# Kernel tuning notes

Hardware: AMD Instinct MI355X
Metric: run time of the kernel (lower is better)

## Reference

```python
import jax, jax.numpy as jnp
import numpy as np

HEADS = 8
DIM_HEAD = 64
SCALE = DIM_HEAD ** -0.5


def setup_inputs() -> dict:
    key = jax.random.key(0)
    ks = jax.random.split(key, 6)
    B, N, D = 1, 4096, 640
    INNER = HEADS * DIM_HEAD  # 512
    s = lambda fan_in: 1.0 / np.sqrt(fan_in)
    return {
        "x": jax.random.normal(ks[0], (B, N, D), dtype=jnp.float32),
        "Wq": jax.random.normal(ks[1], (D, INNER), dtype=jnp.float32) * s(D),
        "Wk": jax.random.normal(ks[2], (D, INNER), dtype=jnp.float32) * s(D),
        "Wv": jax.random.normal(ks[3], (D, INNER), dtype=jnp.float32) * s(D),
        "Wo": jax.random.normal(ks[4], (INNER, D), dtype=jnp.float32) * s(INNER),
        "bo": jnp.zeros((D,), dtype=jnp.float32),
    }


def reference(x, Wq, Wk, Wv, Wo, bo):
    B, N, _ = x.shape
    h, d = HEADS, DIM_HEAD
    # self-attention: context = x
    q = (x @ Wq).reshape(B, N, h, d).transpose(0, 2, 1, 3)  # [B,h,N,d]
    k = (x @ Wk).reshape(B, N, h, d).transpose(0, 2, 1, 3)
    v = (x @ Wv).reshape(B, N, h, d).transpose(0, 2, 1, 3)
    sim = jnp.einsum('bhid,bhjd->bhij', q, k) * SCALE  # [B,h,N,N]
    attn = jax.nn.softmax(sim, axis=-1)
    out = jnp.einsum('bhij,bhjd->bhid', attn, v)  # [B,h,N,d]
    out = out.transpose(0, 2, 1, 3).reshape(B, N, h * d)  # [B,N,inner]
    return out @ Wo + bo  # dropout p=0.0 is identity
```

## Files before the change

kernel.cpp:

```cpp
#include <hip/hip_runtime.h>
#include <math.h>

#define NSEQ   4096
#define DMODEL 640
#define NHEAD  8
#define DHEAD  64
#define INNER  512
#define KVSPLIT 2

typedef _Float16 f16;
typedef _Float16 f16x8 __attribute__((ext_vector_type(8)));
typedef _Float16 f16x4 __attribute__((ext_vector_type(4)));
typedef float    f32x4 __attribute__((ext_vector_type(4)));

#define MFMA16(a, b, c) __builtin_amdgcn_mfma_f32_16x16x32_f16((a), (b), (c), 0, 0, 0)

#define QSCALE 0.18033688011112042f

__device__ __forceinline__ void gl16(const f16* g, f16* l) {
    __builtin_amdgcn_global_load_lds(
        (const __attribute__((address_space(1))) unsigned int*)g,
        (__attribute__((address_space(3))) unsigned int*)l, 16, 0, 0);
}

__global__ __launch_bounds__(256) void cvt_x(const float* __restrict__ x,
                                             f16* __restrict__ xh) {
    int i = (blockIdx.x * 256 + threadIdx.x) * 8;
    float4 a = *(const float4*)&x[i];
    float4 b = *(const float4*)&x[i + 4];
    f16x8 o = {(f16)a.x, (f16)a.y, (f16)a.z, (f16)a.w,
               (f16)b.x, (f16)b.y, (f16)b.z, (f16)b.w};
    *(f16x8*)&xh[i] = o;
}

__global__ __launch_bounds__(256) void transpose_cvtW(
    const float* __restrict__ Wq, const float* __restrict__ Wk,
    const float* __restrict__ Wv, const float* __restrict__ Wo,
    f16* __restrict__ WTq, f16* __restrict__ WTk, f16* __restrict__ WTv,
    f16* __restrict__ WoT) {
    __shared__ __align__(16) f16 T[64][72];
    const int bz = blockIdx.z;
    const float* src = bz == 0 ? Wq : bz == 1 ? Wk : bz == 2 ? Wv : Wo;
    f16* dst = bz == 0 ? WTq : bz == 1 ? WTk : bz == 2 ? WTv : WoT;
    const int R = (bz < 3) ? DMODEL : INNER;
    const int C = (bz < 3) ? INNER : DMODEL;
    const int c0 = blockIdx.x * 64, r0 = blockIdx.y * 64;
    if (c0 >= C || r0 >= R) return;
    const int t = threadIdx.x;
    {
        int r = t >> 2, cb = (t & 3) * 16;
#pragma unroll
        for (int i = 0; i < 16; i += 4) {
            float4 v = *(const float4*)&src[(size_t)(r0 + r) * C + c0 + cb + i];
            T[cb + i + 0][r] = (f16)v.x;
            T[cb + i + 1][r] = (f16)v.y;
            T[cb + i + 2][r] = (f16)v.z;
            T[cb + i + 3][r] = (f16)v.w;
        }
    }
    __syncthreads();
    {
        int c = t >> 2, rb = (t & 3) * 16;
        f16* d = dst + (size_t)(c0 + c) * R + r0 + rb;
        *(f16x8*)d = *(const f16x8*)&T[c][rb];
        *(f16x8*)(d + 8) = *(const f16x8*)&T[c][rb + 8];
    }
}

__global__ __launch_bounds__(256) void qkv_gemm16(
    const f16* __restrict__ xh,
    const f16* __restrict__ WTq, const f16* __restrict__ WTk,
    const f16* __restrict__ WTv,
    f16* __restrict__ q16, f16* __restrict__ k16, f16* __restrict__ vT16)
{
    __shared__ __align__(16) f16 S[12288];
    f16* Xs = S;
    f16* Ws = S + 8192;

    const int bx = blockIdx.x;
    const int by = blockIdx.y;
    const int bz = blockIdx.z;
    const f16* WT = (bz == 0) ? WTq : (bz == 1) ? WTk : WTv;

    const int tid = threadIdx.x;
    const int w = tid >> 6, lane = tid & 63;
    const int lr = lane & 15, lc = lane >> 4;
    const int srow8 = lane >> 3;
    const int le = 8 * ((lane & 7) ^ srow8);
    const int swz0 = 8 * (lc ^ (lr & 7));
    const int swz1 = 8 * ((lc + 4) ^ (lr & 7));
    const int m0 = by * 128, n0 = bx * 64;

    f32x4 acc[2][4] = {};

    for (int s = 0; s < DMODEL / 64; ++s) {
        const int k0 = s * 64;
#pragma unroll
        for (int c = 0; c < 4; ++c) {
            const int cc = 4 * w + c;
            gl16(xh + (size_t)(m0 + cc * 8 + srow8) * DMODEL + k0 + le,
                 &Xs[cc * 512]);
        }
#pragma unroll
        for (int c = 0; c < 2; ++c) {
            const int cc = 2 * w + c;
            gl16(WT + (size_t)(n0 + cc * 8 + srow8) * DMODEL + k0 + le,
                 &Ws[cc * 512]);
        }
        __syncthreads();
        f16x8 a0[2], a1[2];
#pragma unroll
        for (int g = 0; g < 2; ++g) {
            const int row = 32 * w + 16 * g + lr;
            a0[g] = *(const f16x8*)&Xs[row * 64 + swz0];
            a1[g] = *(const f16x8*)&Xs[row * 64 + swz1];
        }
#pragma unroll
        for (int nt = 0; nt < 4; ++nt) {
            f16x8 b0 = *(const f16x8*)&Ws[(nt * 16 + lr) * 64 + swz0];
            f16x8 b1 = *(const f16x8*)&Ws[(nt * 16 + lr) * 64 + swz1];
#pragma unroll
            for (int g = 0; g < 2; ++g)
                acc[g][nt] = MFMA16(a1[g], b1, MFMA16(a0[g], b0, acc[g][nt]));
        }
        __syncthreads();
    }

    const float sc = (bz == 0) ? QSCALE : 1.0f;
    if (bz < 2) {
#pragma unroll
        for (int g = 0; g < 2; ++g)
#pragma unroll
            for (int nt = 0; nt < 4; ++nt)
#pragma unroll
                for (int r = 0; r < 4; ++r)
                    S[(32 * w + 16 * g + 4 * lc + r) * 72 + nt * 16 + lr] =
                        (f16)(acc[g][nt][r] * sc);
        __syncthreads();
        f16* ob = ((bz == 0) ? q16 : k16) + (size_t)bx * NSEQ * DHEAD;
#pragma unroll
        for (int p = 0; p < 2; ++p) {
            const int rr = p * 64 + (tid >> 2), cb = (tid & 3) * 16;
            f16* dst = ob + (size_t)(m0 + rr) * DHEAD + cb;
            *(f16x8*)dst = *(const f16x8*)&S[rr * 72 + cb];
            *(f16x8*)(dst + 8) = *(const f16x8*)&S[rr * 72 + cb + 8];
        }
    } else {
#pragma unroll
        for (int g = 0; g < 2; ++g)
#pragma unroll
            for (int nt = 0; nt < 4; ++nt)
#pragma unroll
                for (int r = 0; r < 4; ++r)
                    S[(nt * 16 + lr) * 136 + 32 * w + 16 * g + 4 * lc + r] =
                        (f16)acc[g][nt][r];
        __syncthreads();
        const int rr = tid >> 2, cb = (tid & 3) * 32;
        f16* dst = vT16 + ((size_t)bx * DHEAD + rr) * NSEQ + m0 + cb;
        *(f16x8*)dst        = *(const f16x8*)&S[rr * 136 + cb];
        *(f16x8*)(dst + 8)  = *(const f16x8*)&S[rr * 136 + cb + 8];
        *(f16x8*)(dst + 16) = *(const f16x8*)&S[rr * 136 + cb + 16];
        *(f16x8*)(dst + 24) = *(const f16x8*)&S[rr * 136 + cb + 24];
    }
}

__global__ __launch_bounds__(256, 2) void attn_fwd(
    const f16* __restrict__ q16, const f16* __restrict__ k16,
    const f16* __restrict__ vT16, f16* __restrict__ Opart,
    float* __restrict__ Ml)
{
    __shared__ __align__(16) f16 KsB[2][4096];
    __shared__ __align__(16) f16 VtB[2][4096];
    __shared__ __align__(16) f16 Ps[8192];

    const int lin = blockIdx.x + 32 * blockIdx.y + 256 * blockIdx.z;
    const int h  = lin & 7;
    const int qb = (lin >> 3) & 31;
    const int sp = lin >> 8;

    const int tid = threadIdx.x;
    const int w = tid >> 6, lane = tid & 63;
    const int lr = lane & 15, lc = lane >> 4;
    const int srow8 = lane >> 3;
    const int le = 8 * ((lane & 7) ^ srow8);
    const int swz0 = 8 * (lc ^ (lr & 7));
    const int swz1 = 8 * ((lc + 4) ^ (lr & 7));

    const f16* kp = k16 + ((size_t)h * NSEQ + sp * (NSEQ / KVSPLIT)) * DHEAD;
    const f16* vp = vT16 + (size_t)h * DHEAD * NSEQ + sp * (NSEQ / KVSPLIT);

    f16x8 qf[2][2];
#pragma unroll
    for (int g = 0; g < 2; ++g) {
        const f16* qp = q16 +
            ((size_t)h * NSEQ + qb * 128 + 32 * w + 16 * g + lr) * DHEAD;
        qf[g][0] = *(const f16x8*)&qp[lc * 8];
        qf[g][1] = *(const f16x8*)&qp[32 + lc * 8];
    }

    float m_run[2] = {-INFINITY, -INFINITY}, l_run[2] = {0.f, 0.f};
    f32x4 o[2][4] = {};

#pragma unroll
    for (int c = 0; c < 2; ++c) {
        const int cc = 2 * w + c;
        gl16(kp + (size_t)(cc * 8 + srow8) * DHEAD + le, &KsB[0][cc * 512]);
        gl16(vp + (size_t)(cc * 8 + srow8) * NSEQ + le, &VtB[0][cc * 512]);
    }
    __syncthreads();

    const int NT = NSEQ / KVSPLIT / 64;
    for (int kt = 0; kt < NT; ++kt) {
        const int cur = kt & 1;
        if (kt < NT - 1) {
            const int nb = cur ^ 1;
#pragma unroll
            for (int c = 0; c < 2; ++c) {
                const int cc = 2 * w + c;
                gl16(kp + (size_t)((kt + 1) * 64 + cc * 8 + srow8) * DHEAD + le,
                     &KsB[nb][cc * 512]);
                gl16(vp + (size_t)(cc * 8 + srow8) * NSEQ + (kt + 1) * 64 + le,
                     &VtB[nb][cc * 512]);
            }
        }

        f32x4 s[2][4];
        const f32x4 z4 = {0.f, 0.f, 0.f, 0.f};
#pragma unroll
        for (int t = 0; t < 4; ++t) {
            f16x8 ka = *(const f16x8*)&KsB[cur][(t * 16 + lr) * 64 + swz0];
            f16x8 kb = *(const f16x8*)&KsB[cur][(t * 16 + lr) * 64 + swz1];
#pragma unroll
            for (int g = 0; g < 2; ++g)
                s[g][t] = MFMA16(kb, qf[g][1], MFMA16(ka, qf[g][0], z4));
        }

        float pm[2];
#pragma unroll
        for (int g = 0; g < 2; ++g) {
            float m = s[g][0][0];
#pragma unroll
            for (int t = 0; t < 4; ++t)
#pragma unroll
                for (int r = 0; r < 4; ++r) m = fmaxf(m, s[g][t][r]);
            m = fmaxf(m, __shfl_xor(m, 16));
            m = fmaxf(m, __shfl_xor(m, 32));
            pm[g] = m;
        }
        if (__any((pm[0] > m_run[0]) | (pm[1] > m_run[1]))) {
#pragma unroll
            for (int g = 0; g < 2; ++g) {
                const float mn = fmaxf(m_run[g], pm[g]);
                const float al = __builtin_amdgcn_exp2f(m_run[g] - mn);
                m_run[g] = mn;
                l_run[g] *= al;
#pragma unroll
                for (int dt = 0; dt < 4; ++dt) o[g][dt] *= al;
            }
        }
#pragma unroll
        for (int g = 0; g < 2; ++g) {
            float ps = 0.f;
#pragma unroll
            for (int t = 0; t < 4; ++t)
#pragma unroll
                for (int r = 0; r < 4; ++r) {
                    s[g][t][r] = __builtin_amdgcn_exp2f(s[g][t][r] - m_run[g]);
                    ps += s[g][t][r];
                }
            ps += __shfl_xor(ps, 16);
            ps += __shfl_xor(ps, 32);
            l_run[g] += ps;
        }

#pragma unroll
        for (int g = 0; g < 2; ++g) {
            const int row = 32 * w + 16 * g + lr;
#pragma unroll
            for (int t = 0; t < 4; ++t) {
                f16x4 pk = {(f16)s[g][t][0], (f16)s[g][t][1],
                            (f16)s[g][t][2], (f16)s[g][t][3]};
                const int col = (16 * t + 4 * lc) ^ ((lr & 7) << 3);
                *(f16x4*)&Ps[row * 64 + col] = pk;
            }
        }

        f16x8 pb[2][2];
#pragma unroll
        for (int g = 0; g < 2; ++g) {
            const int row = 32 * w + 16 * g + lr;
            pb[g][0] = *(const f16x8*)&Ps[row * 64 + swz0];
            pb[g][1] = *(const f16x8*)&Ps[row * 64 + swz1];
        }
#pragma unroll
        for (int dt = 0; dt < 4; ++dt) {
            f16x8 va0 = *(const f16x8*)&VtB[cur][(dt * 16 + lr) * 64 + swz0];
            f16x8 va1 = *(const f16x8*)&VtB[cur][(dt * 16 + lr) * 64 + swz1];
#pragma unroll
            for (int g = 0; g < 2; ++g)
                o[g][dt] = MFMA16(va1, pb[g][1], MFMA16(va0, pb[g][0], o[g][dt]));
        }
        __syncthreads();
    }

#pragma unroll
    for (int g = 0; g < 2; ++g) {
        const float linv = 1.0f / l_run[g];
        const size_t qg = (size_t)qb * 128 + 32 * w + 16 * g + lr;
        f16* ob = Opart + (((size_t)(sp * 8 + h)) * NSEQ + qg) * DHEAD;
#pragma unroll
        for (int dt = 0; dt < 4; ++dt) {
            f16x4 ov = {(f16)(o[g][dt][0] * linv), (f16)(o[g][dt][1] * linv),
                        (f16)(o[g][dt][2] * linv), (f16)(o[g][dt][3] * linv)};
            *(f16x4*)&ob[dt * 16 + 4 * lc] = ov;
        }
        if (lc == 0) {
            float2 ml = make_float2(m_run[g], l_run[g]);
            *(float2*)&Ml[(((size_t)(sp * 8 + h)) * NSEQ + qg) * 2] = ml;
        }
    }
}

__global__ __launch_bounds__(256) void out_gemm16(
    const f16* __restrict__ Opart, const float* __restrict__ Ml,
    const f16* __restrict__ WoT,
    const float* __restrict__ bias, float* __restrict__ C)
{
    __shared__ __align__(16) f16 Xs[4096];
    __shared__ __align__(16) f16 Ws[4096];

    const int bx = blockIdx.x;
    const int by = blockIdx.y;
    const int tid = threadIdx.x;
    const int w = tid >> 6, lane = tid & 63;
    const int lr = lane & 15, lc = lane >> 4;
    const int srow8 = lane >> 3;
    const int j = lane & 7;
    const int le = 8 * (j ^ srow8);
    const int swz0 = 8 * (lc ^ (lr & 7));
    const int swz1 = 8 * ((lc + 4) ^ (lr & 7));
    const int m0 = by * 64, n0 = bx * 64;

    f32x4 acc[4] = {};

    for (int s8 = 0; s8 < 8; ++s8) {
        const int k0 = s8 * 64;
#pragma unroll
        for (int c = 0; c < 2; ++c) {
            const int cc = w * 2 + c;
            gl16(WoT + (size_t)(n0 + cc * 8 + srow8) * INNER + k0 + le,
                 &Ws[cc * 512]);
            const int row = cc * 8 + srow8;
            const size_t q = (size_t)m0 + row;
            f16x8 o0 = *(const f16x8*)&Opart[((size_t)s8 * NSEQ + q) * DHEAD + 8 * j];
            f16x8 o1 = *(const f16x8*)&Opart[((size_t)(8 + s8) * NSEQ + q) * DHEAD + 8 * j];
            float2 ml0 = *(const float2*)&Ml[((size_t)s8 * NSEQ + q) * 2];
            float2 ml1 = *(const float2*)&Ml[((size_t)(8 + s8) * NSEQ + q) * 2];
            const float mx = fmaxf(ml0.x, ml1.x);
            float w0 = ml0.y * __builtin_amdgcn_exp2f(ml0.x - mx);
            float w1 = ml1.y * __builtin_amdgcn_exp2f(ml1.x - mx);
            const float inv = 1.0f / (w0 + w1);
            w0 *= inv; w1 *= inv;
            f16x8 a8;
#pragma unroll
            for (int e = 0; e < 8; ++e)
                a8[e] = (f16)((float)o0[e] * w0 + (float)o1[e] * w1);
            *(f16x8*)&Xs[row * 64 + 8 * (j ^ (row & 7))] = a8;
        }
        __syncthreads();
        f16x8 a0 = *(const f16x8*)&Xs[(16 * w + lr) * 64 + swz0];
        f16x8 a1 = *(const f16x8*)&Xs[(16 * w + lr) * 64 + swz1];
#pragma unroll
        for (int nt = 0; nt < 4; ++nt) {
            f16x8 b0 = *(const f16x8*)&Ws[(nt * 16 + lr) * 64 + swz0];
            f16x8 b1 = *(const f16x8*)&Ws[(nt * 16 + lr) * 64 + swz1];
            acc[nt] = MFMA16(a1, b1, MFMA16(a0, b0, acc[nt]));
        }
        __syncthreads();
    }

#pragma unroll
    for (int nt = 0; nt < 4; ++nt) {
        const float b = bias[n0 + nt * 16 + lr];
#pragma unroll
        for (int r = 0; r < 4; ++r)
            C[(size_t)(m0 + 16 * w + lc * 4 + r) * DMODEL + n0 + nt * 16 + lr] =
                acc[nt][r] + b;
    }
}

extern "C" void kernel_launch(void* const* d_in, const int* in_sizes, int n_in,
                              void* d_out, int out_size, void* d_ws, size_t ws_size,
                              hipStream_t stream) {
    const float* x  = (const float*)d_in[0];
    const float* Wq = (const float*)d_in[1];
    const float* Wk = (const float*)d_in[2];
    const float* Wv = (const float*)d_in[3];
    const float* Wo = (const float*)d_in[4];
    const float* bo = (const float*)d_in[5];
    float* out = (float*)d_out;

    char* base = (char*)d_ws;
    f16*   Opart = (f16*)base;
    f16*   xh    = (f16*)base;
    f16*   WTq   = xh + (size_t)NSEQ * DMODEL;
    f16*   WTk   = WTq + (size_t)INNER * DMODEL;
    f16*   WTv   = WTk + (size_t)INNER * DMODEL;
    float* Ml    = (float*)(base + 8388608);
    f16*   WoT   = (f16*)(base + 8912896);
    f16*   q16   = (f16*)(base + 9568256);
    f16*   k16   = q16 + (size_t)NHEAD * NSEQ * DHEAD;
    f16*   vT16  = k16 + (size_t)NHEAD * NSEQ * DHEAD;

    cvt_x<<<NSEQ * DMODEL / (256 * 8), 256, 0, stream>>>(x, xh);
    transpose_cvtW<<<dim3(10, 10, 4), 256, 0, stream>>>(
        Wq, Wk, Wv, Wo, WTq, WTk, WTv, WoT);

    qkv_gemm16<<<dim3(NHEAD, NSEQ / 128, 3), 256, 0, stream>>>(
        xh, WTq, WTk, WTv, q16, k16, vT16);
    attn_fwd<<<dim3(NSEQ / 128, NHEAD, KVSPLIT), 256, 0, stream>>>(
        q16, k16, vT16, Opart, Ml);
    out_gemm16<<<dim3(DMODEL / 64, NSEQ / 64), 256, 0, stream>>>(
        Opart, Ml, WoT, bo, out);
}
```

Before: 170.0 us.

## Software-pipeline attention loop: overlap QK^T of next tile with softmax/PV of previous

Restructures the flash-attention inner loop so that each iteration computes S=QK^T for tile j while finishing softmax and the PV product for tile j-1, using two register score buffers and a 4-deep V shared-memory ring. The aim is to interleave MFMA work from independent tiles with the exp/reduction VALU work so the two can overlap. In exchange it holds more score registers, which may pressure occupancy at launch_bounds(256,2), and uses more LDS for the extra V buffers.

```diff
diff --git a/kernel.cpp b/kernel.cpp
--- a/kernel.cpp
+++ b/kernel.cpp
@@ -170,7 +170,7 @@
     float* __restrict__ Ml)
 {
     __shared__ __align__(16) f16 KsB[2][4096];
-    __shared__ __align__(16) f16 VtB[2][4096];
+    __shared__ __align__(16) f16 VtB[4][4096];
     __shared__ __align__(16) f16 Ps[8192];
 
     const int lin = blockIdx.x + 32 * blockIdx.y + 256 * blockIdx.z;
@@ -200,108 +200,125 @@
 
     float m_run[2] = {-INFINITY, -INFINITY}, l_run[2] = {0.f, 0.f};
     f32x4 o[2][4] = {};
-
-#pragma unroll
-    for (int c = 0; c < 2; ++c) {
-        const int cc = 2 * w + c;
-        gl16(kp + (size_t)(cc * 8 + srow8) * DHEAD + le, &KsB[0][cc * 512]);
-        gl16(vp + (size_t)(cc * 8 + srow8) * NSEQ + le, &VtB[0][cc * 512]);
-    }
+    f32x4 sA[2][4], sB[2][4];
+    const int NT = NSEQ / KVSPLIT / 64;
+
+#define PREFETCH(J, KB, VB) {                                                 \
+    _Pragma("unroll")                                                         \
+    for (int c = 0; c < 2; ++c) {                                             \
+        const int cc = 2 * w + c;                                             \
+        gl16(kp + (size_t)((J) * 64 + cc * 8 + srow8) * DHEAD + le,           \
+             &KsB[KB][cc * 512]);                                             \
+        gl16(vp + (size_t)(cc * 8 + srow8) * NSEQ + (J) * 64 + le,            \
+             &VtB[VB][cc * 512]);                                             \
+    } }
+
+#define QKT(KB, S) {                                                          \
+    const f32x4 z4 = {0.f, 0.f, 0.f, 0.f};                                    \
+    _Pragma("unroll")                                                         \
+    for (int t = 0; t < 4; ++t) {                                             \
+        f16x8 ka = *(const f16x8*)&KsB[KB][(t * 16 + lr) * 64 + swz0];        \
+        f16x8 kb = *(const f16x8*)&KsB[KB][(t * 16 + lr) * 64 + swz1];        \
+        _Pragma("unroll")                                                     \
+        for (int g = 0; g < 2; ++g)                                           \
+            S[g][t] = MFMA16(kb, qf[g][1], MFMA16(ka, qf[g][0], z4));         \
+    } }
+
+#define FINISH(VB, S) {                                                       \
+    float pm[2];                                                              \
+    _Pragma("unroll")                                                         \
+    for (int g = 0; g < 2; ++g) {                                             \
+        float mm = S[g][0][0];                                                \
+        _Pragma("unroll")                                                     \
+        for (int t = 0; t < 4; ++t)                                           \
+            _Pragma("unroll")                                                 \
+            for (int r = 0; r < 4; ++r) mm = fmaxf(mm, S[g][t][r]);           \
+        mm = fmaxf(mm, __shfl_xor(mm, 16));                                   \
+        mm = fmaxf(mm, __shfl_xor(mm, 32));                                   \
+        pm[g] = mm;                                                           \
+    }                                                                         \
+    if (__any((pm[0] > m_run[0]) | (pm[1] > m_run[1]))) {                     \
+        _Pragma("unroll")                                                     \
+        for (int g = 0; g < 2; ++g) {                                         \
+            const float mn = fmaxf(m_run[g], pm[g]);                          \
+            const float al = __builtin_amdgcn_exp2f(m_run[g] - mn);           \
+            m_run[g] = mn;                                                    \
+            l_run[g] *= al;                                                   \
+            _Pragma("unroll")                                                 \
+            for (int dt = 0; dt < 4; ++dt) o[g][dt] *= al;                    \
+        }                                                                     \
+    }                                                                         \
+    _Pragma("unroll")                                                         \
+    for (int g = 0; g < 2; ++g) {                                             \
+        float ps = 0.f;                                                       \
+        _Pragma("unroll")                                                     \
+        for (int t = 0; t < 4; ++t)                                           \
+            _Pragma("unroll")                                                 \
+            for (int r = 0; r < 4; ++r) {                                     \
+                S[g][t][r] = __builtin_amdgcn_exp2f(S[g][t][r] - m_run[g]);   \
+                ps += S[g][t][r];                                             \
+            }                                                                 \
+        ps += __shfl_xor(ps, 16);                                             \
+        ps += __shfl_xor(ps, 32);                                             \
+        l_run[g] += ps;                                                       \
+    }                                                                         \
+    _Pragma("unroll")                                                         \
+    for (int g = 0; g < 2; ++g) {                                             \
+        const int row = 32 * w + 16 * g + lr;                                 \
+        _Pragma("unroll")                                                     \
+        for (int t = 0; t < 4; ++t) {                                         \
+            f16x4 pk = {(f16)S[g][t][0], (f16)S[g][t][1],                     \
+                        (f16)S[g][t][2], (f16)S[g][t][3]};                    \
+            const int col = (16 * t + 4 * lc) ^ ((lr & 7) << 3);              \
+            *(f16x4*)&Ps[row * 64 + col] = pk;                                \
+        }                                                                     \
+    }                                                                         \
+    {                                                                         \
+        f16x8 pb[2][2];                                                       \
+        _Pragma("unroll")                                                     \
+        for (int g = 0; g < 2; ++g) {                                         \
+            const int row = 32 * w + 16 * g + lr;                             \
+            pb[g][0] = *(const f16x8*)&Ps[row * 64 + swz0];                   \
+            pb[g][1] = *(const f16x8*)&Ps[row * 64 + swz1];                   \
+        }                                                                     \
+        _Pragma("unroll")                                                     \
+        for (int dt = 0; dt < 4; ++dt) {                                      \
+            f16x8 va0 = *(const f16x8*)&VtB[VB][(dt * 16 + lr) * 64 + swz0];  \
+            f16x8 va1 = *(const f16x8*)&VtB[VB][(dt * 16 + lr) * 64 + swz1];  \
+            _Pragma("unroll")                                                 \
+            for (int g = 0; g < 2; ++g)                                       \
+                o[g][dt] = MFMA16(va1, pb[g][1],                              \
+                                  MFMA16(va0, pb[g][0], o[g][dt]));           \
+        }                                                                     \
+    } }
+
+#define BODY(J, U, SCUR, SPRV) {                                              \
+    if ((J) + 1 < NT) PREFETCH((J) + 1, ((U) + 1) & 1, ((U) + 1) & 3);        \
+    QKT((U) & 1, SCUR);                                                       \
+    if ((J) > 0) FINISH(((U) + 3) & 3, SPRV);                                 \
+    __syncthreads();                                                          \
+    }
+
+    PREFETCH(0, 0, 0);
     __syncthreads();
 
-    const int NT = NSEQ / KVSPLIT / 64;
-    for (int kt = 0; kt < NT; ++kt) {
-        const int cur = kt & 1;
-        if (kt < NT - 1) {
-            const int nb = cur ^ 1;
-#pragma unroll
-            for (int c = 0; c < 2; ++c) {
-                const int cc = 2 * w + c;
-                gl16(kp + (size_t)((kt + 1) * 64 + cc * 8 + srow8) * DHEAD + le,
-                     &KsB[nb][cc * 512]);
-                gl16(vp + (size_t)(cc * 8 + srow8) * NSEQ + (kt + 1) * 64 + le,
-                     &VtB[nb][cc * 512]);
-            }
-        }
-
-        f32x4 s[2][4];
-        const f32x4 z4 = {0.f, 0.f, 0.f, 0.f};
-#pragma unroll
-        for (int t = 0; t < 4; ++t) {
-            f16x8 ka = *(const f16x8*)&KsB[cur][(t * 16 + lr) * 64 + swz0];
-            f16x8 kb = *(const f16x8*)&KsB[cur][(t * 16 + lr) * 64 + swz1];
-#pragma unroll
-            for (int g = 0; g < 2; ++g)
-                s[g][t] = MFMA16(kb, qf[g][1], MFMA16(ka, qf[g][0], z4));
-        }
-
-        float pm[2];
-#pragma unroll
-        for (int g = 0; g < 2; ++g) {
-            float m = s[g][0][0];
-#pragma unroll
-            for (int t = 0; t < 4; ++t)
-#pragma unroll
-                for (int r = 0; r < 4; ++r) m = fmaxf(m, s[g][t][r]);
-            m = fmaxf(m, __shfl_xor(m, 16));
-            m = fmaxf(m, __shfl_xor(m, 32));
-            pm[g] = m;
-        }
-        if (__any((pm[0] > m_run[0]) | (pm[1] > m_run[1]))) {
-#pragma unroll
-            for (int g = 0; g < 2; ++g) {
-                const float mn = fmaxf(m_run[g], pm[g]);
-                const float al = __builtin_amdgcn_exp2f(m_run[g] - mn);
-                m_run[g] = mn;
-                l_run[g] *= al;
-#pragma unroll
-                for (int dt = 0; dt < 4; ++dt) o[g][dt] *= al;
-            }
-        }
-#pragma unroll
-        for (int g = 0; g < 2; ++g) {
-            float ps = 0.f;
-#pragma unroll
-            for (int t = 0; t < 4; ++t)
-#pragma unroll
-                for (int r = 0; r < 4; ++r) {
-                    s[g][t][r] = __builtin_amdgcn_exp2f(s[g][t][r] - m_run[g]);
-                    ps += s[g][t][r];
-                }
-            ps += __shfl_xor(ps, 16);
-            ps += __shfl_xor(ps, 32);
-            l_run[g] += ps;
-        }
-
-#pragma unroll
-        for (int g = 0; g < 2; ++g) {
-            const int row = 32 * w + 16 * g + lr;
-#pragma unroll
-            for (int t = 0; t < 4; ++t) {
-                f16x4 pk = {(f16)s[g][t][0], (f16)s[g][t][1],
-                            (f16)s[g][t][2], (f16)s[g][t][3]};
-                const int col = (16 * t + 4 * lc) ^ ((lr & 7) << 3);
-                *(f16x4*)&Ps[row * 64 + col] = pk;
-            }
-        }
-
-        f16x8 pb[2][2];
-#pragma unroll
-        for (int g = 0; g < 2; ++g) {
-            const int row = 32 * w + 16 * g + lr;
-            pb[g][0] = *(const f16x8*)&Ps[row * 64 + swz0];
-            pb[g][1] = *(const f16x8*)&Ps[row * 64 + swz1];
-        }
-#pragma unroll
-        for (int dt = 0; dt < 4; ++dt) {
-            f16x8 va0 = *(const f16x8*)&VtB[cur][(dt * 16 + lr) * 64 + swz0];
-            f16x8 va1 = *(const f16x8*)&VtB[cur][(dt * 16 + lr) * 64 + swz1];
-#pragma unroll
-            for (int g = 0; g < 2; ++g)
-                o[g][dt] = MFMA16(va1, pb[g][1], MFMA16(va0, pb[g][0], o[g][dt]));
-        }
-        __syncthreads();
-    }
+    BODY(0, 0, sA, sB);
+    BODY(1, 1, sB, sA);
+    BODY(2, 2, sA, sB);
+    BODY(3, 3, sB, sA);
+    for (int m = 1; m < 8; ++m) {
+        const int j = 4 * m;
+        BODY(j, 0, sA, sB);
+        BODY(j + 1, 1, sB, sA);
+        BODY(j + 2, 2, sA, sB);
+        BODY(j + 3, 3, sB, sA);
+    }
+    FINISH(3, sB);
+
+#undef BODY
+#undef FINISH
+#undef QKT
+#undef PREFETCH
 
 #pragma unroll
     for (int g = 0; g < 2; ++g) {
```

Result: faster. 164.1 us (-3.5%).
